# Kernel optimization log

Hardware: AMD Instinct MI355X
Metric: run time of the kernel (lower is better)

Reference implementation:

```python
import jax, jax.numpy as jnp
import numpy as np

B, N, E, R = 2, 4096, 1024, 128   # batch, seq_len, embed_dim, expand_ratio (head_dim)
H = E // R                        # num heads (scalar decay per head)
EPS = 1e-5                        # torch LayerNorm default eps


def _silu(x):
    return x * jax.nn.sigmoid(x)


def setup_inputs() -> dict:
    key = jax.random.key(0)
    ks = jax.random.split(key, 12)
    std = 0.02

    def w(k, shape):
        return jax.random.normal(k, shape, jnp.float32) * std

    return {
        "x": jax.random.normal(ks[0], (B, N, E), jnp.float32),
        # log of lower bound of the decay gate; must be negative so exp() in (0,1)
        "log_lower_bound": -jax.random.uniform(ks[1], (H,), jnp.float32, minval=0.1, maxval=3.0),
        "Wq": w(ks[2], (E, E)),
        "Wk": w(ks[3], (E, E)),
        "Wv": w(ks[4], (E, E)),
        "Wf": w(ks[5], (H, E)),      # f_proj: embed_dim -> embed_dim // expand_ratio
        "Wb1": w(ks[6], (R, E)),     # bet_proj low-rank
        "Wb2": w(ks[7], (E, R)),
        "Wg1": w(ks[8], (R, E)),     # output_gate low-rank
        "Wg2": w(ks[9], (E, R)),
        "gamma": jnp.ones((E,), jnp.float32),  # LayerNorm weight (bias=False)
        "Wo": w(ks[10], (E, E)),
    }


def _simple_gla(q, k, v, g):
    """Gated linear attention recurrence (fla simple_gla semantics).
    q,k,v: [B,H,N,R]; g: [B,H,N] (log decay per head per step).
    S_t = exp(g_t) * S_{t-1} + k_t v_t^T ;  o_t = (q_t * d^-0.5) @ S_t
    """
    scale = q.shape[-1] ** -0.5
    qT = jnp.moveaxis(q, 2, 0)  # [N,B,H,R]
    kT = jnp.moveaxis(k, 2, 0)
    vT = jnp.moveaxis(v, 2, 0)
    gT = jnp.moveaxis(g, 2, 0)  # [N,B,H]

    S0 = jnp.zeros((q.shape[0], q.shape[1], q.shape[-1], v.shape[-1]), q.dtype)

    def step(S, inp):
        qt, kt, vt, gt = inp
        S = S * jnp.exp(gt)[..., None, None] + kt[..., :, None] * vt[..., None, :]
        o = jnp.einsum('bhk,bhkv->bhv', qt * scale, S)
        return S, o

    _, o = jax.lax.scan(step, S0, (qT, kT, vT, gT))
    return jnp.moveaxis(o, 0, 2)  # [B,H,N,R]


def reference(x, log_lower_bound, Wq, Wk, Wv, Wf, Wb1, Wb2, Wg1, Wg2, gamma, Wo):
    # projections + activations
    q = _silu(x @ Wq.T)
    k = _silu(x @ Wk.T)
    v = x @ Wv.T
    f = x @ Wf.T                      # [B,N,H] scalar decay logits per head

    # householder q-transform with dense-memory beta (normalized reflection vector)
    beta = _silu((x @ Wb1.T) @ Wb2.T)  # [B,N,E]
    bn = beta * jax.lax.rsqrt(jnp.sum(beta * beta, -1, keepdims=True) + 1e-12)
    q = q - 2.0 * jnp.sum(q * bn, -1, keepdims=True) * bn

    def split_heads(t):  # [B,N,E] -> [B,H,N,R]
        return jnp.moveaxis(t.reshape(B, N, H, R), 2, 1)

    qh, kh, vh = split_heads(q), split_heads(k), split_heads(v)

    # log-space decay gate with lower bound
    lb = jnp.exp(log_lower_bound)                      # [H] in (0,1)
    fg = lb + (1.0 - lb) * jax.nn.sigmoid(f)           # [B,N,H]
    log_f = jnp.transpose(jnp.log(fg), (0, 2, 1))      # [B,H,N]

    o = _simple_gla(qh, kh, vh, log_f)                 # [B,H,N,R]
    o = jnp.moveaxis(o, 1, 2).reshape(B, N, E)

    # output gate
    gate = jax.nn.sigmoid((x @ Wg1.T) @ Wg2.T)
    o = o * gate

    # LayerNorm (weight only, bias=False)
    mu = jnp.mean(o, -1, keepdims=True)
    var = jnp.mean((o - mu) ** 2, -1, keepdims=True)
    o = (o - mu) * jax.lax.rsqrt(var + EPS) * gamma

    return o @ Wo.T
```

## Files before the change

### kernel.cpp

```cpp
#include <hip/hip_runtime.h>
#include <hip/hip_bf16.h>

using u16 = unsigned short;
typedef __attribute__((ext_vector_type(8))) short bf16x8;
typedef __attribute__((ext_vector_type(4))) float f32x4;
typedef __attribute__((ext_vector_type(8))) u16 u16x8;
typedef __attribute__((ext_vector_type(4))) u16 u16x4;

#define B_ 2
#define N_ 4096
#define E_ 1024
#define R_ 128
#define H_ 8
#define M_ 8192
#define CHUNK_ 128
#define NC_ 32
#define BH_ 16

__device__ __forceinline__ float b2f(u16 u) { return __uint_as_float(((unsigned)u) << 16); }
__device__ __forceinline__ u16 f2b(float f) {
  unsigned u = __float_as_uint(f);
  return (u16)((u + 0x7fffu + ((u >> 16) & 1u)) >> 16);
}
__device__ __forceinline__ float sigm(float x) { return 1.0f / (1.0f + expf(-x)); }

#define GLDS(g, l) __builtin_amdgcn_global_load_lds( \
    (const __attribute__((address_space(1))) unsigned int*)(g), \
    (__attribute__((address_space(3))) unsigned int*)(l), 16, 0, 0)

struct CvtArgs {
  const float* src[10];
  u16* dst[11];
};

__global__ void __launch_bounds__(256) cvt_all(CvtArgs a) {
  int idx = blockIdx.x * 256 + threadIdx.x;
  const int SZ[11] = {2097152, 262144, 262144, 262144, 2048,
                      32768, 32768, 32768, 32768, 262144, 30720};
  int off = idx, seg = 0;
#pragma unroll
  for (int i = 0; i < 10; i++) {
    if (seg == i && off >= SZ[i]) { off -= SZ[i]; seg = i + 1; }
  }
  u16x4 z = (u16x4){0, 0, 0, 0};
  if (seg == 10) { ((u16x4*)a.dst[10])[off] = z; return; }
  float4 v = ((const float4*)a.src[seg])[off];
  u16x4 r;
  r[0] = f2b(v.x); r[1] = f2b(v.y); r[2] = f2b(v.z); r[3] = f2b(v.w);
  if (seg == 6) {
    int n = off >> 5, c = off & 31;
    u16x4* W2 = (u16x4*)a.dst[6];
    W2[n * 64 + c] = r; W2[n * 64 + 32 + c] = z;
  } else if (seg == 8) {
    int n = off >> 5, c = off & 31;
    u16x4* W2 = (u16x4*)a.dst[8];
    W2[(1024 + n) * 64 + 32 + c] = r; W2[(1024 + n) * 64 + c] = z;
  } else {
    ((u16x4*)a.dst[seg])[off] = r;
  }
}

__device__ __forceinline__ void mfma_panel(f32x4 (&acc)[4][4], const u16* A, const u16* Bm,
                                           int wr, int wc, int l15, int q8) {
  bf16x8 af[4], bf[4];
#pragma unroll
  for (int mi = 0; mi < 4; mi++) af[mi] = *(const bf16x8*)&A[(wr * 64 + mi * 16 + l15) * 32 + q8];
#pragma unroll
  for (int ni = 0; ni < 4; ni++) bf[ni] = *(const bf16x8*)&Bm[(wc * 64 + ni * 16 + l15) * 32 + q8];
#pragma unroll
  for (int mi = 0; mi < 4; mi++)
#pragma unroll
    for (int ni = 0; ni < 4; ni++)
      acc[mi][ni] = __builtin_amdgcn_mfma_f32_16x16x32_bf16(af[mi], bf[ni], acc[mi][ni], 0, 0, 0);
}

__device__ __forceinline__ void gemm_loop(const u16* __restrict__ X, const u16* __restrict__ W,
                                          int m0, int n0, int K,
                                          u16* As, u16* Bs, f32x4 (&acc)[4][4], int tid) {
  const int wave = tid >> 6, lane = tid & 63;
  const int wr = wave >> 1, wc = wave & 1, l15 = lane & 15, q8 = (lane >> 4) * 8;
  const u16* Ap = X + (size_t)(m0 + wave * 32 + (lane >> 2)) * K + (lane & 3) * 8;
  const u16* Bp = W + (size_t)(n0 + wave * 32 + (lane >> 2)) * K + (lane & 3) * 8;
  u16* A0 = As + wave * 1024;
  u16* B0 = Bs + wave * 1024;
  for (int k0 = 0; k0 < K; k0 += 64) {
    GLDS(Ap + k0,                    A0);
    GLDS(Ap + 16 * (size_t)K + k0,   A0 + 512);
    GLDS(Ap + k0 + 32,               A0 + 4096);
    GLDS(Ap + 16 * (size_t)K + k0 + 32, A0 + 4608);
    GLDS(Bp + k0,                    B0);
    GLDS(Bp + 16 * (size_t)K + k0,   B0 + 512);
    GLDS(Bp + k0 + 32,               B0 + 4096);
    GLDS(Bp + 16 * (size_t)K + k0 + 32, B0 + 4608);
    __syncthreads();
    mfma_panel(acc, As, Bs, wr, wc, l15, q8);
    mfma_panel(acc, As + 4096, Bs + 4096, wr, wc, l15, q8);
    __syncthreads();
  }
}

__global__ void __launch_bounds__(256) mega_gemm(const u16* __restrict__ X, const u16* __restrict__ Wcat,
                                                 const float* __restrict__ llb,
                                                 u16* __restrict__ Qb, u16* __restrict__ Kb,
                                                 u16* __restrict__ KT, u16* __restrict__ VT,
                                                 u16* __restrict__ T1, float* __restrict__ LOGF) {
  __shared__ u16 As[8192];
  __shared__ u16 Bs[8192];
  const int tid = threadIdx.x;
  const int m0 = blockIdx.x * 128;
  const int ny = blockIdx.y, n0 = ny * 128;
  f32x4 acc[4][4];
#pragma unroll
  for (int i = 0; i < 4; i++)
#pragma unroll
    for (int j = 0; j < 4; j++) acc[i][j] = (f32x4){0.f, 0.f, 0.f, 0.f};
  gemm_loop(X, Wcat, m0, n0, 1024, As, Bs, acc, tid);

  const int wave = tid >> 6, lane = tid & 63;
  const int wr = wave >> 1, wc = wave & 1, l15 = lane & 15, q4 = (lane >> 4) * 4;
#pragma unroll
  for (int mi = 0; mi < 4; mi++) {
#pragma unroll
    for (int ni = 0; ni < 4; ni++) {
      int col = n0 + wc * 64 + ni * 16 + l15;
      int rbase = m0 + wr * 64 + mi * 16 + q4;
      float vv[4];
#pragma unroll
      for (int r = 0; r < 4; r++) vv[r] = acc[mi][ni][r];
      if (ny < 16) {
#pragma unroll
        for (int r = 0; r < 4; r++) vv[r] = vv[r] * sigm(vv[r]);
      }
      if (ny < 8) {
#pragma unroll
        for (int r = 0; r < 4; r++) Qb[(size_t)(rbase + r) * E_ + col] = f2b(vv[r]);
      } else if (ny < 16) {
        int ck = col - 1024;
#pragma unroll
        for (int r = 0; r < 4; r++) Kb[(size_t)(rbase + r) * E_ + ck] = f2b(vv[r]);
        int bb = rbase >> 12, n = rbase & (N_ - 1);
        size_t tidx = ((size_t)(bb * H_ + (ck >> 7)) * R_ + (ck & (R_ - 1))) * N_ + n;
        u16x4 pk;
#pragma unroll
        for (int r = 0; r < 4; r++) pk[r] = f2b(vv[r]);
        *(u16x4*)&KT[tidx] = pk;
      } else if (ny < 24) {
        int cv = col - 2048;
        int bb = rbase >> 12, n = rbase & (N_ - 1);
        size_t tidx = ((size_t)(bb * H_ + (cv >> 7)) * R_ + (cv & (R_ - 1))) * N_ + n;
        u16x4 pk;
#pragma unroll
        for (int r = 0; r < 4; r++) pk[r] = f2b(vv[r]);
        *(u16x4*)&VT[tidx] = pk;
      } else if (ny < 26) {
        int ct = col - 3072;
#pragma unroll
        for (int r = 0; r < 4; r++) T1[(size_t)(rbase + r) * 256 + ct] = f2b(vv[r]);
      } else if (wc == 0 && ni == 0 && l15 < 8) {
        int h = l15, bb = rbase >> 12, n = rbase & (N_ - 1);
        float lb = expf(llb[h]);
        float4 o;
        o.x = logf(lb + (1.f - lb) * sigm(vv[0]));
        o.y = logf(lb + (1.f - lb) * sigm(vv[1]));
        o.z = logf(lb + (1.f - lb) * sigm(vv[2]));
        o.w = logf(lb + (1.f - lb) * sigm(vv[3]));
        *(float4*)&LOGF[(size_t)(bb * H_ + h) * N_ + n] = o;
      }
    }
  }
}

__global__ void __launch_bounds__(256) bg_gemm(const u16* __restrict__ T1, const u16* __restrict__ W2,
                                               u16* __restrict__ BETA, u16* __restrict__ GATE) {
  __shared__ u16 As[8192];
  __shared__ u16 Bs[8192];
  const int tid = threadIdx.x;
  const int m0 = blockIdx.x * 128;
  const int n0 = blockIdx.y * 128;
  f32x4 acc[4][4];
#pragma unroll
  for (int i = 0; i < 4; i++)
#pragma unroll
    for (int j = 0; j < 4; j++) acc[i][j] = (f32x4){0.f, 0.f, 0.f, 0.f};
  gemm_loop(T1, W2, m0, n0, 256, As, Bs, acc, tid);
  const int wave = tid >> 6, lane = tid & 63;
  const int wr = wave >> 1, wc = wave & 1, l15 = lane & 15, q4 = (lane >> 4) * 4;
#pragma unroll
  for (int mi = 0; mi < 4; mi++) {
#pragma unroll
    for (int ni = 0; ni < 4; ni++) {
      int col = n0 + wc * 64 + ni * 16 + l15;
      int rbase = m0 + wr * 64 + mi * 16 + q4;
      if (col < 1024) {
#pragma unroll
        for (int r = 0; r < 4; r++) {
          float v = acc[mi][ni][r];
          BETA[(size_t)(rbase + r) * E_ + col] = f2b(v * sigm(v));
        }
      } else {
#pragma unroll
        for (int r = 0; r < 4; r++)
          GATE[(size_t)(rbase + r) * E_ + col - 1024] = f2b(sigm(acc[mi][ni][r]));
      }
    }
  }
}

__global__ void __launch_bounds__(256) out_gemm(const u16* __restrict__ X, const u16* __restrict__ W,
                                                float* __restrict__ C) {
  __shared__ u16 As[8192];
  __shared__ u16 Bs[8192];
  const int tid = threadIdx.x;
  const int m0 = blockIdx.x * 128;
  const int n0 = blockIdx.y * 128;
  f32x4 acc[4][4];
#pragma unroll
  for (int i = 0; i < 4; i++)
#pragma unroll
    for (int j = 0; j < 4; j++) acc[i][j] = (f32x4){0.f, 0.f, 0.f, 0.f};
  gemm_loop(X, W, m0, n0, 1024, As, Bs, acc, tid);
  const int wave = tid >> 6, lane = tid & 63;
  const int wr = wave >> 1, wc = wave & 1, l15 = lane & 15, q4 = (lane >> 4) * 4;
#pragma unroll
  for (int mi = 0; mi < 4; mi++) {
#pragma unroll
    for (int ni = 0; ni < 4; ni++) {
      int col = n0 + wc * 64 + ni * 16 + l15;
      int rbase = m0 + wr * 64 + mi * 16 + q4;
#pragma unroll
      for (int r = 0; r < 4; r++)
        C[(size_t)(rbase + r) * E_ + col] = acc[mi][ni][r];
    }
  }
}

__global__ void __launch_bounds__(256) householder(u16* __restrict__ Q, const u16* __restrict__ BETA) {
  int row = blockIdx.x;
  int tid = threadIdx.x;
  u16* q = Q + (size_t)row * E_;
  const u16* bt = BETA + (size_t)row * E_;
  u16x4 q4 = *(const u16x4*)(q + tid * 4);
  u16x4 b4 = *(const u16x4*)(bt + tid * 4);
  float qv[4], bv[4];
#pragma unroll
  for (int i = 0; i < 4; i++) { qv[i] = b2f(q4[i]); bv[i] = b2f(b4[i]); }
  float ss = bv[0]*bv[0] + bv[1]*bv[1] + bv[2]*bv[2] + bv[3]*bv[3];
  float qd = qv[0]*bv[0] + qv[1]*bv[1] + qv[2]*bv[2] + qv[3]*bv[3];
  __shared__ float red[8];
#pragma unroll
  for (int m = 1; m < 64; m <<= 1) { ss += __shfl_xor(ss, m); qd += __shfl_xor(qd, m); }
  int wid = tid >> 6;
  if ((tid & 63) == 0) { red[wid] = ss; red[4 + wid] = qd; }
  __syncthreads();
  ss = red[0] + red[1] + red[2] + red[3];
  qd = red[4] + red[5] + red[6] + red[7];
  float coef = 2.f * qd / (ss + 1e-12f);
  const float scale = 0.08838834764831845f;
  u16x4 o4;
#pragma unroll
  for (int i = 0; i < 4; i++) o4[i] = f2b((qv[i] - coef * bv[i]) * scale);
  *(u16x4*)(q + tid * 4) = o4;
}

__device__ __forceinline__ void scan_chunk(const float* __restrict__ lf, float* cum, int tid) {
  if (tid < 64) {
    float a = lf[tid], b = lf[tid + 64];
#pragma unroll
    for (int off = 1; off < 64; off <<= 1) {
      float t = __shfl_up(a, off);  if (tid >= off) a += t;
      float t2 = __shfl_up(b, off); if (tid >= off) b += t2;
    }
    b += __shfl(a, 63);
    cum[tid] = a; cum[tid + 64] = b;
  }
  __syncthreads();
}

__device__ __forceinline__ void stage32(u16* dst, const u16* src, size_t stride, int tid) {
  int r0 = tid >> 2, c8 = (tid & 3) * 8;
  *(u16x8*)&dst[(size_t)r0 * 40 + c8] = *(const u16x8*)&src[(size_t)r0 * stride + c8];
  int r1 = r0 + 64;
  *(u16x8*)&dst[(size_t)r1 * 40 + c8] = *(const u16x8*)&src[(size_t)r1 * stride + c8];
}

__device__ __forceinline__ void stage32_scaled(u16* dst, const u16* src, size_t stride,
                                               const float* w, int j0, int tid) {
  int c8 = (tid & 3) * 8;
  float wv[8];
#pragma unroll
  for (int i = 0; i < 8; i++) wv[i] = w[j0 + c8 + i];
#pragma unroll
  for (int rr = 0; rr < 128; rr += 64) {
    int r = rr + (tid >> 2);
    u16x8 raw = *(const u16x8*)&src[(size_t)r * stride + c8];
    u16x8 o;
#pragma unroll
    for (int i = 0; i < 8; i++) o[i] = f2b(b2f(raw[i]) * wv[i]);
    *(u16x8*)&dst[(size_t)r * 40 + c8] = o;
  }
}

__device__ __forceinline__ void mfma16(f32x4 (&acc)[4][4], const u16* A, const u16* Bm,
                                       int wr, int wc, int l15, int q8) {
  bf16x8 af[4], bf[4];
#pragma unroll
  for (int mi = 0; mi < 4; mi++) af[mi] = *(const bf16x8*)&A[(wr * 64 + mi * 16 + l15) * 40 + q8];
#pragma unroll
  for (int ni = 0; ni < 4; ni++) bf[ni] = *(const bf16x8*)&Bm[(wc * 64 + ni * 16 + l15) * 40 + q8];
#pragma unroll
  for (int mi = 0; mi < 4; mi++)
#pragma unroll
    for (int ni = 0; ni < 4; ni++)
      acc[mi][ni] = __builtin_amdgcn_mfma_f32_16x16x32_bf16(af[mi], bf[ni], acc[mi][ni], 0, 0, 0);
}

__global__ void __launch_bounds__(256) gla_phaseA(const u16* __restrict__ KT, const u16* __restrict__ VT,
                                                  const float* __restrict__ LOGF,
                                                  float* __restrict__ U, float* __restrict__ DC) {
  const int blk = blockIdx.x;
  const int bh = blk >> 5, c = blk & 31;
  const int tid = threadIdx.x;
  const int wave = tid >> 6, lane = tid & 63;
  const int wr = wave >> 1, wc = wave & 1, l15 = lane & 15, q8 = (lane >> 4) * 8;
  __shared__ u16 SA[128 * 40];
  __shared__ u16 SB[128 * 40];
  __shared__ float cum[CHUNK_];
  __shared__ float wd[CHUNK_];
  scan_chunk(LOGF + (size_t)bh * N_ + c * CHUNK_, cum, tid);
  if (tid < 128) wd[tid] = expf(cum[127] - cum[tid]);
  __syncthreads();
  const u16* vbase = VT + ((size_t)bh * R_) * N_ + (size_t)c * CHUNK_;
  const u16* kbase = KT + ((size_t)bh * R_) * N_ + (size_t)c * CHUNK_;
  f32x4 acc[4][4];
#pragma unroll
  for (int i = 0; i < 4; i++)
#pragma unroll
    for (int j = 0; j < 4; j++) acc[i][j] = (f32x4){0.f, 0.f, 0.f, 0.f};
  for (int j0 = 0; j0 < CHUNK_; j0 += 32) {
    __syncthreads();
    stage32(SA, vbase + j0, N_, tid);
    stage32_scaled(SB, kbase + j0, N_, wd, j0, tid);
    __syncthreads();
    mfma16(acc, SA, SB, wr, wc, l15, q8);
  }
  float* Up = U + (size_t)blk * (R_ * R_);
#pragma unroll
  for (int mi = 0; mi < 4; mi++) {
#pragma unroll
    for (int ni = 0; ni < 4; ni++) {
      int v = wr * 64 + mi * 16 + (lane >> 4) * 4;
      int k = wc * 64 + ni * 16 + l15;
#pragma unroll
      for (int r = 0; r < 4; r++) Up[(size_t)(v + r) * R_ + k] = acc[mi][ni][r];
    }
  }
  if (tid == 0) DC[blk] = expf(cum[127]);
}

__global__ void __launch_bounds__(256) gla_phaseB(const float* __restrict__ U, const float* __restrict__ DC,
                                                  u16* __restrict__ SSb) {
  int idx = blockIdx.x * 256 + threadIdx.x;
  int bh = idx >> 14;
  int e = idx & 16383;
  float s = 0.f;
  for (int c = 0; c < NC_; c++) {
    size_t off = ((size_t)bh * NC_ + c) * 16384 + e;
    SSb[off] = f2b(s);
    s = DC[bh * NC_ + c] * s + U[off];
  }
}

__global__ void __launch_bounds__(256) gla_phaseC(const u16* __restrict__ Qb, const u16* __restrict__ Kb,
                                                  const u16* __restrict__ VT, const u16* __restrict__ SSb,
                                                  const float* __restrict__ LOGF, u16* __restrict__ Ob) {
  const int blk = blockIdx.x;
  const int bh = blk >> 5, c = blk & 31;
  const int b = bh >> 3, h = bh & 7;
  const int tid = threadIdx.x;
  const int wave = tid >> 6, lane = tid & 63;
  const int wr = wave >> 1, wc = wave & 1, l15 = lane & 15;
  const int q4i = (lane >> 4) * 4, q8 = (lane >> 4) * 8;
  __shared__ u16 SA[128 * 40];
  __shared__ u16 SB[128 * 40];
  __shared__ u16 Ps[128 * 136];
  __shared__ float cum[CHUNK_];
  __shared__ float cumE[CHUNK_];
  scan_chunk(LOGF + (size_t)bh * N_ + c * CHUNK_, cum, tid);
  if (tid < 128) cumE[tid] = expf(cum[tid]);
  __syncthreads();
  const size_t rowbase = ((size_t)(b * N_ + c * CHUNK_)) * E_ + (size_t)h * R_;
  const u16* vtbase = VT + ((size_t)bh * R_) * N_ + (size_t)c * CHUNK_;
  const u16* ssbase = SSb + (size_t)blk * (R_ * R_);

  f32x4 acc[4][4];
#pragma unroll
  for (int i = 0; i < 4; i++)
#pragma unroll
    for (int j = 0; j < 4; j++) acc[i][j] = (f32x4){0.f, 0.f, 0.f, 0.f};

  for (int r0 = 0; r0 < R_; r0 += 32) {
    __syncthreads();
    stage32(SA, Kb + rowbase + r0, E_, tid);
    stage32(SB, Qb + rowbase + r0, E_, tid);
    __syncthreads();
    mfma16(acc, SA, SB, wr, wc, l15, q8);
  }
#pragma unroll
  for (int mi = 0; mi < 4; mi++) {
#pragma unroll
    for (int ni = 0; ni < 4; ni++) {
      int jb = wr * 64 + mi * 16 + q4i;
      int i = wc * 64 + ni * 16 + l15;
      float ci = cum[i];
      float4 cj = *(const float4*)&cum[jb];
      u16x4 pk;
      float cjv[4] = {cj.x, cj.y, cj.z, cj.w};
#pragma unroll
      for (int r = 0; r < 4; r++) {
        int j = jb + r;
        float w = (j <= i) ? expf(ci - cjv[r]) : 0.f;
        pk[r] = f2b(acc[mi][ni][r] * w);
      }
      *(u16x4*)&Ps[i * 136 + jb] = pk;
    }
  }
#pragma unroll
  for (int i = 0; i < 4; i++)
#pragma unroll
    for (int j = 0; j < 4; j++) acc[i][j] = (f32x4){0.f, 0.f, 0.f, 0.f};
  for (int k0 = 0; k0 < R_; k0 += 32) {
    __syncthreads();
    stage32(SA, Qb + rowbase + k0, E_, tid);
    stage32(SB, ssbase + k0, R_, tid);
    __syncthreads();
    mfma16(acc, SA, SB, wr, wc, l15, q8);
  }
#pragma unroll
  for (int mi = 0; mi < 4; mi++) {
    float4 e4 = *(const float4*)&cumE[wr * 64 + mi * 16 + q4i];
    float ev[4] = {e4.x, e4.y, e4.z, e4.w};
#pragma unroll
    for (int ni = 0; ni < 4; ni++)
#pragma unroll
      for (int r = 0; r < 4; r++) acc[mi][ni][r] *= ev[r];
  }
  for (int j0 = 0; j0 < CHUNK_; j0 += 32) {
    __syncthreads();
    stage32(SB, vtbase + j0, N_, tid);
    __syncthreads();
    if (wr == 1 || j0 < 64) {
      bf16x8 af[4], bf[4];
#pragma unroll
      for (int mi = 0; mi < 4; mi++)
        af[mi] = *(const bf16x8*)&Ps[(wr * 64 + mi * 16 + l15) * 136 + j0 + q8];
#pragma unroll
      for (int ni = 0; ni < 4; ni++)
        bf[ni] = *(const bf16x8*)&SB[(wc * 64 + ni * 16 + l15) * 40 + q8];
#pragma unroll
      for (int mi = 0; mi < 4; mi++)
#pragma unroll
        for (int ni = 0; ni < 4; ni++)
          acc[mi][ni] = __builtin_amdgcn_mfma_f32_16x16x32_bf16(af[mi], bf[ni], acc[mi][ni], 0, 0, 0);
    }
  }
#pragma unroll
  for (int mi = 0; mi < 4; mi++) {
#pragma unroll
    for (int ni = 0; ni < 4; ni++) {
      int i = wr * 64 + mi * 16 + q4i;
      int v = wc * 64 + ni * 16 + l15;
#pragma unroll
      for (int r = 0; r < 4; r++)
        Ob[rowbase + (size_t)(i + r) * E_ + v] = f2b(acc[mi][ni][r]);
    }
  }
}

__global__ void __launch_bounds__(256) gate_ln(const u16* __restrict__ O, const u16* __restrict__ G,
                                               const float* __restrict__ gamma, u16* __restrict__ OLN) {
  int row = blockIdx.x, tid = threadIdx.x;
  u16x4 o4 = *(const u16x4*)(O + (size_t)row * E_ + tid * 4);
  u16x4 g4 = *(const u16x4*)(G + (size_t)row * E_ + tid * 4);
  float x0 = b2f(o4[0]) * b2f(g4[0]), x1 = b2f(o4[1]) * b2f(g4[1]);
  float x2 = b2f(o4[2]) * b2f(g4[2]), x3 = b2f(o4[3]) * b2f(g4[3]);
  float s = x0 + x1 + x2 + x3;
  float sq = x0 * x0 + x1 * x1 + x2 * x2 + x3 * x3;
  __shared__ float red[8];
#pragma unroll
  for (int m = 1; m < 64; m <<= 1) { s += __shfl_xor(s, m); sq += __shfl_xor(sq, m); }
  int wid = tid >> 6;
  if ((tid & 63) == 0) { red[wid] = s; red[4 + wid] = sq; }
  __syncthreads();
  s = red[0] + red[1] + red[2] + red[3];
  sq = red[4] + red[5] + red[6] + red[7];
  float mu = s * (1.f / 1024.f);
  float var = sq * (1.f / 1024.f) - mu * mu;
  float rs = rsqrtf(var + 1e-5f);
  int e = tid * 4;
  u16x4 r4;
  r4[0] = f2b((x0 - mu) * rs * gamma[e + 0]);
  r4[1] = f2b((x1 - mu) * rs * gamma[e + 1]);
  r4[2] = f2b((x2 - mu) * rs * gamma[e + 2]);
  r4[3] = f2b((x3 - mu) * rs * gamma[e + 3]);
  *(u16x4*)(OLN + (size_t)row * E_ + e) = r4;
}

extern "C" void kernel_launch(void* const* d_in, const int* in_sizes, int n_in,
                              void* d_out, int out_size, void* d_ws, size_t ws_size,
                              hipStream_t stream) {
  (void)in_sizes; (void)n_in; (void)out_size; (void)ws_size;
  const float* x   = (const float*)d_in[0];
  const float* llb = (const float*)d_in[1];
  const float* Wq  = (const float*)d_in[2];
  const float* Wk  = (const float*)d_in[3];
  const float* Wv  = (const float*)d_in[4];
  const float* Wf  = (const float*)d_in[5];
  const float* Wb1 = (const float*)d_in[6];
  const float* Wb2 = (const float*)d_in[7];
  const float* Wg1 = (const float*)d_in[8];
  const float* Wg2 = (const float*)d_in[9];
  const float* gm  = (const float*)d_in[10];
  const float* Wo  = (const float*)d_in[11];
  float* out = (float*)d_out;

  char* ws = (char*)d_ws;
  const size_t SZB = (size_t)M_ * E_ * 2;
  u16*   Qb    = (u16*)(ws + 0 * SZB);
  u16*   Kb    = (u16*)(ws + 1 * SZB);
  u16*   KT    = (u16*)(ws + 2 * SZB);
  u16*   VT    = (u16*)(ws + 3 * SZB);
  u16*   BETAb = (u16*)(ws + 4 * SZB);
  u16*   GATEb = (u16*)(ws + 5 * SZB);
  u16*   SSb   = (u16*)(ws + 6 * SZB);
  u16*   XB    = (u16*)(ws + 7 * SZB);
  float* U     = (float*)(ws + 8 * SZB);
  char*  tail  = ws + 8 * SZB + (size_t)BH_ * NC_ * R_ * R_ * 4;
  u16*   Wcat  = (u16*)tail;
  u16*   Wcat2 = Wcat + (size_t)3456 * 1024;
  u16*   WOb   = Wcat2 + (size_t)2048 * 256;
  u16*   T1    = WOb + (size_t)E_ * E_;
  float* LOGF  = (float*)(T1 + (size_t)M_ * 256);
  float* DC    = LOGF + (size_t)BH_ * N_;
  u16*   Ob    = BETAb;
  u16*   OLN   = Qb;

  CvtArgs ca;
  ca.src[0] = x;   ca.dst[0]  = XB;
  ca.src[1] = Wq;  ca.dst[1]  = Wcat;
  ca.src[2] = Wk;  ca.dst[2]  = Wcat + (size_t)1024 * 1024;
  ca.src[3] = Wv;  ca.dst[3]  = Wcat + (size_t)2048 * 1024;
  ca.src[4] = Wf;  ca.dst[4]  = Wcat + (size_t)3328 * 1024;
  ca.src[5] = Wb1; ca.dst[5]  = Wcat + (size_t)3072 * 1024;
  ca.src[6] = Wb2; ca.dst[6]  = Wcat2;
  ca.src[7] = Wg1; ca.dst[7]  = Wcat + (size_t)3200 * 1024;
  ca.src[8] = Wg2; ca.dst[8]  = Wcat2;
  ca.src[9] = Wo;  ca.dst[9]  = WOb;
  ca.dst[10] = Wcat + (size_t)3336 * 1024;

  dim3 blk(256);
  cvt_all<<<dim3(12928), blk, 0, stream>>>(ca);
  mega_gemm<<<dim3(64, 27), blk, 0, stream>>>(XB, Wcat, llb, Qb, Kb, KT, VT, T1, LOGF);
  bg_gemm<<<dim3(64, 16), blk, 0, stream>>>(T1, Wcat2, BETAb, GATEb);
  householder<<<dim3(M_), blk, 0, stream>>>(Qb, BETAb);
  gla_phaseA<<<dim3(BH_ * NC_), blk, 0, stream>>>(KT, VT, LOGF, U, DC);
  gla_phaseB<<<dim3(BH_ * 16384 / 256), blk, 0, stream>>>(U, DC, SSb);
  gla_phaseC<<<dim3(BH_ * NC_), blk, 0, stream>>>(Qb, Kb, VT, SSb, LOGF, Ob);
  gate_ln<<<dim3(M_), blk, 0, stream>>>(Ob, GATEb, gm, OLN);
  out_gemm<<<dim3(64, 8), blk, 0, stream>>>(OLN, WOb, out);
}
```

Baseline: 343.5 us.

## Stage K/V transposes through LDS for coalesced stores and use fast intrinsics

The mega_gemm epilogue now writes the K and V tiles into shared memory first, then stores the transposed layouts with 16-byte coalesced row writes instead of scattered 8-byte stores. Branches are split per output type so each block follows one uniform path, and the log-decay block exits early. Sigmoid, exp and log now use hardware approximate intrinsics (rcp, __expf, __logf) throughout. This trades some accuracy and a little extra shared memory for fewer scattered global writes and cheaper transcendentals.

```diff
diff --git a/kernel.cpp b/kernel.cpp
--- a/kernel.cpp
+++ b/kernel.cpp
@@ -22,7 +22,9 @@
   unsigned u = __float_as_uint(f);
   return (u16)((u + 0x7fffu + ((u >> 16) & 1u)) >> 16);
 }
-__device__ __forceinline__ float sigm(float x) { return 1.0f / (1.0f + expf(-x)); }
+__device__ __forceinline__ float sigm(float x) {
+  return __builtin_amdgcn_rcpf(1.0f + __expf(-x));
+}
 
 #define GLDS(g, l) __builtin_amdgcn_global_load_lds( \
     (const __attribute__((address_space(1))) unsigned int*)(g), \
@@ -104,8 +106,10 @@
                                                  u16* __restrict__ Qb, u16* __restrict__ Kb,
                                                  u16* __restrict__ KT, u16* __restrict__ VT,
                                                  u16* __restrict__ T1, float* __restrict__ LOGF) {
-  __shared__ u16 As[8192];
-  __shared__ u16 Bs[8192];
+  __shared__ u16 sh[16896];
+  u16* As = sh;
+  u16* Bs = sh + 8192;
+  u16* Ts = sh;
   const int tid = threadIdx.x;
   const int m0 = blockIdx.x * 128;
   const int ny = blockIdx.y, n0 = ny * 128;
@@ -118,54 +122,92 @@
 
   const int wave = tid >> 6, lane = tid & 63;
   const int wr = wave >> 1, wc = wave & 1, l15 = lane & 15, q4 = (lane >> 4) * 4;
-#pragma unroll
-  for (int mi = 0; mi < 4; mi++) {
-#pragma unroll
-    for (int ni = 0; ni < 4; ni++) {
-      int col = n0 + wc * 64 + ni * 16 + l15;
-      int rbase = m0 + wr * 64 + mi * 16 + q4;
-      float vv[4];
-#pragma unroll
-      for (int r = 0; r < 4; r++) vv[r] = acc[mi][ni][r];
-      if (ny < 16) {
-#pragma unroll
-        for (int r = 0; r < 4; r++) vv[r] = vv[r] * sigm(vv[r]);
-      }
-      if (ny < 8) {
-#pragma unroll
-        for (int r = 0; r < 4; r++) Qb[(size_t)(rbase + r) * E_ + col] = f2b(vv[r]);
-      } else if (ny < 16) {
-        int ck = col - 1024;
-#pragma unroll
-        for (int r = 0; r < 4; r++) Kb[(size_t)(rbase + r) * E_ + ck] = f2b(vv[r]);
-        int bb = rbase >> 12, n = rbase & (N_ - 1);
-        size_t tidx = ((size_t)(bb * H_ + (ck >> 7)) * R_ + (ck & (R_ - 1))) * N_ + n;
-        u16x4 pk;
-#pragma unroll
-        for (int r = 0; r < 4; r++) pk[r] = f2b(vv[r]);
-        *(u16x4*)&KT[tidx] = pk;
-      } else if (ny < 24) {
-        int cv = col - 2048;
-        int bb = rbase >> 12, n = rbase & (N_ - 1);
-        size_t tidx = ((size_t)(bb * H_ + (cv >> 7)) * R_ + (cv & (R_ - 1))) * N_ + n;
-        u16x4 pk;
-#pragma unroll
-        for (int r = 0; r < 4; r++) pk[r] = f2b(vv[r]);
-        *(u16x4*)&VT[tidx] = pk;
-      } else if (ny < 26) {
-        int ct = col - 3072;
-#pragma unroll
-        for (int r = 0; r < 4; r++) T1[(size_t)(rbase + r) * 256 + ct] = f2b(vv[r]);
-      } else if (wc == 0 && ni == 0 && l15 < 8) {
+
+  if (ny == 26) {
+#pragma unroll
+    for (int mi = 0; mi < 4; mi++) {
+      if (wc == 0 && l15 < 8) {
+        int rbase = m0 + wr * 64 + mi * 16 + q4;
         int h = l15, bb = rbase >> 12, n = rbase & (N_ - 1);
-        float lb = expf(llb[h]);
+        float lb = __expf(llb[h]);
         float4 o;
-        o.x = logf(lb + (1.f - lb) * sigm(vv[0]));
-        o.y = logf(lb + (1.f - lb) * sigm(vv[1]));
-        o.z = logf(lb + (1.f - lb) * sigm(vv[2]));
-        o.w = logf(lb + (1.f - lb) * sigm(vv[3]));
+        o.x = __logf(lb + (1.f - lb) * sigm(acc[mi][0][0]));
+        o.y = __logf(lb + (1.f - lb) * sigm(acc[mi][0][1]));
+        o.z = __logf(lb + (1.f - lb) * sigm(acc[mi][0][2]));
+        o.w = __logf(lb + (1.f - lb) * sigm(acc[mi][0][3]));
         *(float4*)&LOGF[(size_t)(bb * H_ + h) * N_ + n] = o;
       }
+    }
+    return;
+  }
+
+  u16 pk[4][4][4];
+#pragma unroll
+  for (int mi = 0; mi < 4; mi++)
+#pragma unroll
+    for (int ni = 0; ni < 4; ni++)
+#pragma unroll
+      for (int r = 0; r < 4; r++) {
+        float v = acc[mi][ni][r];
+        if (ny < 16) v = v * sigm(v);
+        pk[mi][ni][r] = f2b(v);
+      }
+
+  if (ny < 8) {
+#pragma unroll
+    for (int mi = 0; mi < 4; mi++)
+#pragma unroll
+      for (int ni = 0; ni < 4; ni++) {
+        int col = n0 + wc * 64 + ni * 16 + l15;
+        int rbase = m0 + wr * 64 + mi * 16 + q4;
+#pragma unroll
+        for (int r = 0; r < 4; r++) Qb[(size_t)(rbase + r) * E_ + col] = pk[mi][ni][r];
+      }
+  } else if (ny < 16) {
+#pragma unroll
+    for (int mi = 0; mi < 4; mi++)
+#pragma unroll
+      for (int ni = 0; ni < 4; ni++) {
+        int col = n0 - 1024 + wc * 64 + ni * 16 + l15;
+        int rbase = m0 + wr * 64 + mi * 16 + q4;
+#pragma unroll
+        for (int r = 0; r < 4; r++) Kb[(size_t)(rbase + r) * E_ + col] = pk[mi][ni][r];
+      }
+  } else if (ny >= 24) {
+#pragma unroll
+    for (int mi = 0; mi < 4; mi++)
+#pragma unroll
+      for (int ni = 0; ni < 4; ni++) {
+        int ct = n0 - 3072 + wc * 64 + ni * 16 + l15;
+        int rbase = m0 + wr * 64 + mi * 16 + q4;
+#pragma unroll
+        for (int r = 0; r < 4; r++) T1[(size_t)(rbase + r) * 256 + ct] = pk[mi][ni][r];
+      }
+    return;
+  }
+
+  if (ny < 24) {
+#pragma unroll
+    for (int mi = 0; mi < 4; mi++)
+#pragma unroll
+      for (int ni = 0; ni < 4; ni++) {
+        int cl = wc * 64 + ni * 16 + l15;
+        int rl = wr * 64 + mi * 16 + q4;
+        u16x4 w4 = {pk[mi][ni][0], pk[mi][ni][1], pk[mi][ni][2], pk[mi][ni][3]};
+        *(u16x4*)&Ts[cl * 132 + rl] = w4;
+      }
+    __syncthreads();
+    u16* TB = (ny < 16) ? KT : VT;
+    int cbase = n0 - ((ny < 16) ? 1024 : 2048);
+    int head = cbase >> 7;
+    int bb = m0 >> 12, nloc = m0 & (N_ - 1);
+    size_t base = ((size_t)(bb * H_ + head) * R_) * N_ + nloc;
+#pragma unroll
+    for (int p = 0; p < 8; p++) {
+      int cl = p * 16 + (tid >> 4);
+      int r8 = (tid & 15) * 8;
+      u16x8 v = *(const u16x8*)&Ts[cl * 132 + r8];
+      *(u16x8*)&TB[base + (size_t)cl * N_ + r8] = v;
     }
   }
 }
@@ -327,7 +369,7 @@
   __shared__ float cum[CHUNK_];
   __shared__ float wd[CHUNK_];
   scan_chunk(LOGF + (size_t)bh * N_ + c * CHUNK_, cum, tid);
-  if (tid < 128) wd[tid] = expf(cum[127] - cum[tid]);
+  if (tid < 128) wd[tid] = __expf(cum[127] - cum[tid]);
   __syncthreads();
   const u16* vbase = VT + ((size_t)bh * R_) * N_ + (size_t)c * CHUNK_;
   const u16* kbase = KT + ((size_t)bh * R_) * N_ + (size_t)c * CHUNK_;
@@ -354,7 +396,7 @@
       for (int r = 0; r < 4; r++) Up[(size_t)(v + r) * R_ + k] = acc[mi][ni][r];
     }
   }
-  if (tid == 0) DC[blk] = expf(cum[127]);
+  if (tid == 0) DC[blk] = __expf(cum[127]);
 }
 
 __global__ void __launch_bounds__(256) gla_phaseB(const float* __restrict__ U, const float* __restrict__ DC,
@@ -386,7 +428,7 @@
   __shared__ float cum[CHUNK_];
   __shared__ float cumE[CHUNK_];
   scan_chunk(LOGF + (size_t)bh * N_ + c * CHUNK_, cum, tid);
-  if (tid < 128) cumE[tid] = expf(cum[tid]);
+  if (tid < 128) cumE[tid] = __expf(cum[tid]);
   __syncthreads();
   const size_t rowbase = ((size_t)(b * N_ + c * CHUNK_)) * E_ + (size_t)h * R_;
   const u16* vtbase = VT + ((size_t)bh * R_) * N_ + (size_t)c * CHUNK_;
@@ -418,7 +460,7 @@
 #pragma unroll
       for (int r = 0; r < 4; r++) {
         int j = jb + r;
-        float w = (j <= i) ? expf(ci - cjv[r]) : 0.f;
+        float w = (j <= i) ? __expf(ci - cjv[r]) : 0.f;
         pk[r] = f2b(acc[mi][ni][r] * w);
       }
       *(u16x4*)&Ps[i * 136 + jb] = pk;
```

Result: faster. 317.8 us (-7.5%).
